# Kernel tuning notes

Measured on AMD Instinct MI355X. Metric: run time of the kernel, lower is better.

Reference implementation:

```python
import jax, jax.numpy as jnp
import numpy as np

WIN = 8          # window size
P = 32           # patch grid side (patch_w_num)
SHIFTS = (0, 4)  # stride=[0,4] -> regular + shifted window branches
HEADS = 16
DH = 64          # dim_head
DIM = 512
HP = HEADS // len(SHIFTS)   # heads per shift branch
NW = (P // WIN) ** 2        # windows per image (16)
WS = WIN * WIN              # tokens per window (64)


def _rel_index():
    c = np.stack(np.meshgrid(np.arange(WIN), np.arange(WIN), indexing="ij")).reshape(2, -1)
    r = (c[:, :, None] - c[:, None, :]).transpose(1, 2, 0) + WIN - 1
    return (r[..., 0] * (2 * WIN - 1) + r[..., 1]).astype(np.int32)  # [WS, WS]

REL_IDX = _rel_index()


def _shift_mask(shift):
    # standard Swin attention mask for cyclic shift
    img = np.zeros((P, P), np.int32); cnt = 0
    sl = (slice(0, -WIN), slice(-WIN, -shift), slice(-shift, None))
    for hs in sl:
        for ws_ in sl:
            img[hs, ws_] = cnt; cnt += 1
    m = img.reshape(P // WIN, WIN, P // WIN, WIN).transpose(0, 2, 1, 3).reshape(NW, WS)
    return np.where(m[:, None, :] != m[:, :, None], -1e9, 0.0).astype(np.float32)  # [NW, WS, WS]

MASK4 = _shift_mask(4)


def _part(t):
    # [B,P,P,hp,dh] -> [B*NW, hp, WS, dh]
    B, _, _, hp, dh = t.shape
    t = t.reshape(B, P // WIN, WIN, P // WIN, WIN, hp, dh)
    t = t.transpose(0, 1, 3, 2, 4, 5, 6).reshape(B * NW, WS, hp, dh)
    return t.transpose(0, 2, 1, 3)


def _merge(t, B):
    # [B*NW, hp, WS, dh] -> [B,P,P,hp,dh]
    hp, dh = t.shape[1], t.shape[3]
    t = t.transpose(0, 2, 1, 3).reshape(B, P // WIN, P // WIN, WIN, WIN, hp, dh)
    return t.transpose(0, 1, 3, 2, 4, 5, 6).reshape(B, P, P, hp, dh)


def setup_inputs() -> dict:
    key = jax.random.key(0)
    ks = jax.random.split(key, 5)
    B = 64
    x = jax.random.normal(ks[0], (B, P * P, DIM), jnp.float32)
    w_qkv = jax.random.normal(ks[1], (DIM, 3 * HEADS * DH), jnp.float32) * (DIM ** -0.5)
    bias_table = jax.random.normal(ks[2], ((2 * WIN - 1) ** 2, HEADS), jnp.float32) * 0.02
    w_out = jax.random.normal(ks[3], (HEADS * DH, DIM), jnp.float32) * ((HEADS * DH) ** -0.5)
    b_out = jnp.zeros((DIM,), jnp.float32)
    return {"x": x, "w_qkv": w_qkv, "bias_table": bias_table, "w_out": w_out, "b_out": b_out}


def reference(x, w_qkv, bias_table, w_out, b_out):
    B, N, _ = x.shape
    scale = DH ** -0.5
    qkv = (x @ w_qkv).reshape(B, P, P, 3, HEADS, DH)
    q, k, v = qkv[..., 0, :, :], qkv[..., 1, :, :], qkv[..., 2, :, :]  # [B,P,P,HEADS,DH]
    bias = bias_table[REL_IDX].transpose(2, 0, 1)  # [HEADS, WS, WS]
    mask4 = jnp.asarray(MASK4)
    outs = []
    for i, shift in enumerate(SHIFTS):
        hs = slice(i * HP, (i + 1) * HP)
        qi, ki, vi = q[..., hs, :], k[..., hs, :], v[..., hs, :]
        if shift:
            qi = jnp.roll(qi, (-shift, -shift), axis=(1, 2))
            ki = jnp.roll(ki, (-shift, -shift), axis=(1, 2))
            vi = jnp.roll(vi, (-shift, -shift), axis=(1, 2))
        qw, kw, vw = _part(qi), _part(ki), _part(vi)  # [B*NW, HP, WS, DH]
        attn = jnp.einsum("whid,whjd->whij", qw * scale, kw) + bias[hs][None]
        if shift:
            attn = attn.reshape(B, NW, HP, WS, WS) + mask4[None, :, None]
            attn = attn.reshape(B * NW, HP, WS, WS)
        attn = jax.nn.softmax(attn, axis=-1)
        ow = jnp.einsum("whij,whjd->whid", attn, vw)
        oi = _merge(ow, B)
        if shift:
            oi = jnp.roll(oi, (shift, shift), axis=(1, 2))
        outs.append(oi)
    out = jnp.concatenate(outs, axis=3).reshape(B, N, HEADS * DH)
    return out @ w_out + b_out
```

## Files before the change

### kernel.cpp

```cpp
#include <hip/hip_runtime.h>
#include <hip/hip_bf16.h>


typedef __attribute__((ext_vector_type(4))) float f32x4;
typedef __attribute__((ext_vector_type(8))) __bf16 bf16x8;
typedef __attribute__((ext_vector_type(8))) unsigned short u16x8;

__device__ __forceinline__ unsigned short f2bf(float f) {
  __hip_bfloat16 h = __float2bfloat16(f);
  return __builtin_bit_cast(unsigned short, h);
}
__device__ __forceinline__ float bf2f(unsigned short u) {
  return __builtin_bit_cast(float, ((unsigned int)u) << 16);
}

#define GLL16(gsrc, ldst)                                                              \
  __builtin_amdgcn_global_load_lds((const __attribute__((address_space(1))) void*)(gsrc), \
                                   (__attribute__((address_space(3))) void*)(ldst), 16, 0, 0)

__global__ __launch_bounds__(256) void cvt_x_kernel(const float* __restrict__ in,
                                                    unsigned short* __restrict__ out, int n4) {
  int i = blockIdx.x * blockDim.x + threadIdx.x;
  int stride = gridDim.x * blockDim.x;
  for (; i < n4; i += stride) {
    float4 v = reinterpret_cast<const float4*>(in)[i];
    ushort4 o;
    o.x = f2bf(v.x); o.y = f2bf(v.y); o.z = f2bf(v.z); o.w = f2bf(v.w);
    reinterpret_cast<ushort4*>(out)[i] = o;
  }
}

__global__ __launch_bounds__(256) void cvt_T_kernel(const float* __restrict__ in,
                                                    unsigned short* __restrict__ out,
                                                    int R, int C) {
  int idx = blockIdx.x * 256 + threadIdx.x;
  if (idx < R * C) {
    int r = idx / C, c = idx - r * C;
    out[(size_t)c * R + r] = f2bf(in[idx]);
  }
}

template <bool OUT_BF16>
__global__ __launch_bounds__(256) void gemm_bt(const unsigned short* __restrict__ A, int lda,
                                               const unsigned short* __restrict__ B, int ldb,
                                               void* __restrict__ Cv, int ldc,
                                               const float* __restrict__ bias,
                                               int N, int K) {
  __shared__ alignas(16) unsigned short As[128 * 32];
  __shared__ alignas(16) unsigned short Bs[128 * 32];
  const int tid = threadIdx.x;
  const int lane = tid & 63;
  const int wave = tid >> 6;
  const int nbn = N >> 7;
  const int nwg = gridDim.x;
  const int b0 = blockIdx.x;
  const int swz = (b0 & 7) * (nwg >> 3) + (b0 >> 3);
  const int bm = swz / nbn, bn = swz - bm * nbn;
  const int m0 = bm << 7, n0 = bn << 7;
  const int wm = (wave >> 1) << 6;
  const int wn = (wave & 1) << 6;
  const int r0 = lane & 15, kh = lane >> 4;

  const int e0 = (wave * 2 + 0) * 512 + lane * 8;
  const int e1 = (wave * 2 + 1) * 512 + lane * 8;
  const int ra0 = e0 >> 5, ca0 = e0 & 31;
  const int ra1 = e1 >> 5, ca1 = e1 & 31;

  f32x4 acc[4][4] = {};
  const int nkt = K >> 5;
  for (int kt = 0; kt < nkt; ++kt) {
    const int k0 = kt << 5;
    if (kt) __syncthreads();
    GLL16(A + (size_t)(m0 + ra0) * lda + k0 + ca0, &As[(wave * 2 + 0) * 512]);
    GLL16(A + (size_t)(m0 + ra1) * lda + k0 + ca1, &As[(wave * 2 + 1) * 512]);
    GLL16(B + (size_t)(n0 + ra0) * ldb + k0 + ca0, &Bs[(wave * 2 + 0) * 512]);
    GLL16(B + (size_t)(n0 + ra1) * ldb + k0 + ca1, &Bs[(wave * 2 + 1) * 512]);
    __syncthreads();
    bf16x8 af[4], bfr[4];
#pragma unroll
    for (int mi = 0; mi < 4; ++mi)
      af[mi] = *reinterpret_cast<const bf16x8*>(&As[(wm + mi * 16 + r0) * 32 + kh * 8]);
#pragma unroll
    for (int ni = 0; ni < 4; ++ni)
      bfr[ni] = *reinterpret_cast<const bf16x8*>(&Bs[(wn + ni * 16 + r0) * 32 + kh * 8]);
#pragma unroll
    for (int mi = 0; mi < 4; ++mi)
#pragma unroll
      for (int ni = 0; ni < 4; ++ni)
        acc[mi][ni] =
            __builtin_amdgcn_mfma_f32_16x16x32_bf16(af[mi], bfr[ni], acc[mi][ni], 0, 0, 0);
  }
  const int rr = kh << 2;
#pragma unroll
  for (int mi = 0; mi < 4; ++mi)
#pragma unroll
    for (int ni = 0; ni < 4; ++ni) {
      const int col = n0 + wn + ni * 16 + r0;
#pragma unroll
      for (int r = 0; r < 4; ++r) {
        const size_t row = (size_t)(m0 + wm + mi * 16 + rr + r);
        if (OUT_BF16)
          ((unsigned short*)Cv)[row * ldc + col] = f2bf(acc[mi][ni][r]);
        else
          ((float*)Cv)[row * ldc + col] = acc[mi][ni][r] + bias[col];
      }
    }
}

__device__ __forceinline__ int region_of(int wy, int wx, int t) {
  int yr = wy * 8 + (t >> 3);
  int xr = wx * 8 + (t & 7);
  int ry = (yr < 24) ? 0 : ((yr < 28) ? 1 : 2);
  int rx = (xr < 24) ? 0 : ((xr < 28) ? 1 : 2);
  return ry * 3 + rx;
}

__global__ __launch_bounds__(256) void win_attn(const unsigned short* __restrict__ qkv,
                                                const float* __restrict__ bias_table,
                                                unsigned short* __restrict__ out,
                                                int nb16) {
  __shared__ alignas(16) unsigned short vt[4][64][72];
  __shared__ alignas(16) unsigned short pl[4][64][72];
  __shared__ unsigned short bias_sh[225 * 16];

  const int tid = threadIdx.x, lane = tid & 63, wave = tid >> 6;
  const int bid = blockIdx.x;
  const int g = bid / nb16;
  const int bw = bid - g * nb16;
  const int b = bw >> 4, w = bw & 15;
  const int wy = w >> 2, wx = w & 3;
  const int shift = g ? 4 : 0;

  for (int i = tid; i < 225 * 16; i += 256) bias_sh[i] = f2bf(bias_table[i]);
  __syncthreads();

  const int r0 = lane & 15, hi4 = lane >> 4;

  for (int hh = 0; hh < 2; ++hh) {
    const int head = g * 8 + wave * 2 + hh;
    const int qcol = head * 64;

    bf16x8 qf[4][2], kf[4][2];
#pragma unroll
    for (int mi = 0; mi < 4; ++mi) {
      const int t = mi * 16 + r0;
      const int y = (wy * 8 + (t >> 3) + shift) & 31;
      const int x = (wx * 8 + (t & 7) + shift) & 31;
      const size_t base = (size_t)((b << 10) + (y << 5) + x) * 3072 + qcol;
#pragma unroll
      for (int kb = 0; kb < 2; ++kb) {
        const int d = kb * 32 + hi4 * 8;
        qf[mi][kb] = *reinterpret_cast<const bf16x8*>(&qkv[base + d]);
        kf[mi][kb] = *reinterpret_cast<const bf16x8*>(&qkv[base + 1024 + d]);
      }
    }

    {
      const int y = (wy * 8 + (lane >> 3) + shift) & 31;
      const int x = (wx * 8 + (lane & 7) + shift) & 31;
      const unsigned short* vsrc =
          qkv + (size_t)((b << 10) + (y << 5) + x) * 3072 + 2048 + qcol;
#pragma unroll
      for (int d0 = 0; d0 < 8; ++d0) {
        u16x8 vv = *reinterpret_cast<const u16x8*>(&vsrc[d0 * 8]);
#pragma unroll
        for (int jj = 0; jj < 8; ++jj) vt[wave][d0 * 8 + jj][lane] = vv[jj];
      }
    }

    f32x4 s[4][4] = {};
#pragma unroll
    for (int mi = 0; mi < 4; ++mi)
#pragma unroll
      for (int ni = 0; ni < 4; ++ni) {
        s[mi][ni] = __builtin_amdgcn_mfma_f32_16x16x32_bf16(qf[mi][0], kf[ni][0], s[mi][ni], 0, 0, 0);
        s[mi][ni] = __builtin_amdgcn_mfma_f32_16x16x32_bf16(qf[mi][1], kf[ni][1], s[mi][ni], 0, 0, 0);
      }

    int rj[4];
#pragma unroll
    for (int ni = 0; ni < 4; ++ni) rj[ni] = region_of(wy, wx, ni * 16 + r0);
    float rinv[4][4];
#pragma unroll
    for (int mi = 0; mi < 4; ++mi) {
#pragma unroll
      for (int r = 0; r < 4; ++r) {
        const int it = mi * 16 + hi4 * 4 + r;
        const int iy = it >> 3, ix = it & 7;
        const int ri = region_of(wy, wx, it);
        float vals[4], vmax = -1e30f;
#pragma unroll
        for (int ni = 0; ni < 4; ++ni) {
          const int jt = ni * 16 + r0;
          const int ridx = (iy - (jt >> 3) + 7) * 15 + (ix - (jt & 7) + 7);
          float v = s[mi][ni][r] * 0.125f + bf2f(bias_sh[ridx * 16 + head]);
          if (g && ri != rj[ni]) v = -1e9f;
          vals[ni] = v;
          vmax = fmaxf(vmax, v);
        }
        vmax = fmaxf(vmax, __shfl_xor(vmax, 1));
        vmax = fmaxf(vmax, __shfl_xor(vmax, 2));
        vmax = fmaxf(vmax, __shfl_xor(vmax, 4));
        vmax = fmaxf(vmax, __shfl_xor(vmax, 8));
        float ssum = 0.f;
#pragma unroll
        for (int ni = 0; ni < 4; ++ni) {
          float p = __expf(vals[ni] - vmax);
          ssum += p;
          s[mi][ni][r] = p;
        }
        ssum += __shfl_xor(ssum, 1);
        ssum += __shfl_xor(ssum, 2);
        ssum += __shfl_xor(ssum, 4);
        ssum += __shfl_xor(ssum, 8);
        rinv[mi][r] = 1.0f / ssum;
      }
    }

#pragma unroll
    for (int mi = 0; mi < 4; ++mi)
#pragma unroll
      for (int ni = 0; ni < 4; ++ni)
#pragma unroll
        for (int r = 0; r < 4; ++r)
          pl[wave][mi * 16 + hi4 * 4 + r][ni * 16 + r0] = f2bf(s[mi][ni][r]);

    f32x4 o[4][4] = {};
#pragma unroll
    for (int kb = 0; kb < 2; ++kb) {
      bf16x8 pf[4], vf[4];
#pragma unroll
      for (int mi = 0; mi < 4; ++mi)
        pf[mi] = *reinterpret_cast<const bf16x8*>(&pl[wave][mi * 16 + r0][kb * 32 + hi4 * 8]);
#pragma unroll
      for (int di = 0; di < 4; ++di)
        vf[di] = *reinterpret_cast<const bf16x8*>(&vt[wave][di * 16 + r0][kb * 32 + hi4 * 8]);
#pragma unroll
      for (int mi = 0; mi < 4; ++mi)
#pragma unroll
        for (int di = 0; di < 4; ++di)
          o[mi][di] = __builtin_amdgcn_mfma_f32_16x16x32_bf16(pf[mi], vf[di], o[mi][di], 0, 0, 0);
    }

#pragma unroll
    for (int mi = 0; mi < 4; ++mi)
#pragma unroll
      for (int r = 0; r < 4; ++r) {
        const int it = mi * 16 + hi4 * 4 + r;
        const int y = (wy * 8 + (it >> 3) + shift) & 31;
        const int x = (wx * 8 + (it & 7) + shift) & 31;
        unsigned short* op = out + (size_t)((b << 10) + (y << 5) + x) * 3072 + head * 64;
        const float rv = rinv[mi][r];
#pragma unroll
        for (int di = 0; di < 4; ++di) op[di * 16 + r0] = f2bf(o[mi][di][r] * rv);
      }
  }
}

extern "C" void kernel_launch(void* const* d_in, const int* in_sizes, int n_in,
                              void* d_out, int out_size, void* d_ws, size_t ws_size,
                              hipStream_t stream) {
  const float* x = (const float*)d_in[0];
  const float* w_qkv = (const float*)d_in[1];
  const float* bias_table = (const float*)d_in[2];
  const float* w_out = (const float*)d_in[3];
  const float* b_out = (const float*)d_in[4];
  float* out = (float*)d_out;

  int S = 1;
  for (; S < 16; S <<= 1) {
    size_t need = 2ull * (2097152ull + 234881024ull / (size_t)S);
    if (need <= ws_size) break;
  }
  const int Mc = 65536 / S;
  const int nb = 64 / S;

  unsigned short* wqt = (unsigned short*)d_ws;
  unsigned short* wot = wqt + (size_t)1572864;
  unsigned short* xb  = wot + (size_t)524288;
  unsigned short* qkv = xb + (size_t)Mc * 512;

  cvt_T_kernel<<<6144, 256, 0, stream>>>(w_qkv, wqt, 512, 3072);
  cvt_T_kernel<<<2048, 256, 0, stream>>>(w_out, wot, 1024, 512);

  for (int c = 0; c < S; ++c) {
    const float* xc = x + (size_t)c * Mc * 512;
    cvt_x_kernel<<<2048, 256, 0, stream>>>(xc, xb, Mc * 128);
    gemm_bt<true><<<(Mc >> 7) * 24, 256, 0, stream>>>(xb, 512, wqt, 512, (void*)qkv, 3072,
                                                      nullptr, 3072, 512);
    win_attn<<<2 * nb * 16, 256, 0, stream>>>(qkv, bias_table, qkv, nb * 16);
    gemm_bt<false><<<(Mc >> 7) * 4, 256, 0, stream>>>(qkv, 3072, wot, 1024,
                                                      (void*)(out + (size_t)c * Mc * 512), 512,
                                                      b_out, 512, 1024);
  }
}
```

Before: 648.4 us.

## Replace GEMM with 256x256 tile, 8-wave, double-buffered pipelined kernel

Replaces the simple 128x128 single-buffered GEMM with a 256x256-tile, 512-thread kernel. It uses a 64-wide K step, double-buffered LDS with XOR swizzling, staged global-to-LDS prefetches interleaved with MFMA phases, and s_setprio around the math. The aim is to raise data reuse, overlap memory loads with compute, and avoid LDS bank conflicts in both projection GEMMs. In exchange it uses 128KB of LDS per block and fewer, larger blocks, which could lower occupancy and raise tail effects on small chunks. The ordering of waitcnt and barriers is delicate.

Result: faster. 592.4 us (-8.6%).

```diff
diff --git a/kernel.cpp b/kernel.cpp
--- a/kernel.cpp
+++ b/kernel.cpp
@@ -17,6 +17,10 @@
 #define GLL16(gsrc, ldst)                                                              \
   __builtin_amdgcn_global_load_lds((const __attribute__((address_space(1))) void*)(gsrc), \
                                    (__attribute__((address_space(3))) void*)(ldst), 16, 0, 0)
+
+#define SWZ(x) ((x) ^ ((((x) >> 9) & 1) << 5))
+
+#define MFMA_BF16 __builtin_amdgcn_mfma_f32_16x16x32_bf16
 
 __global__ __launch_bounds__(256) void cvt_x_kernel(const float* __restrict__ in,
                                                     unsigned short* __restrict__ out, int n4) {
@@ -41,64 +45,143 @@
 }
 
 template <bool OUT_BF16>
-__global__ __launch_bounds__(256) void gemm_bt(const unsigned short* __restrict__ A, int lda,
-                                               const unsigned short* __restrict__ B, int ldb,
-                                               void* __restrict__ Cv, int ldc,
-                                               const float* __restrict__ bias,
-                                               int N, int K) {
-  __shared__ alignas(16) unsigned short As[128 * 32];
-  __shared__ alignas(16) unsigned short Bs[128 * 32];
-  const int tid = threadIdx.x;
-  const int lane = tid & 63;
-  const int wave = tid >> 6;
-  const int nbn = N >> 7;
+__global__ __launch_bounds__(512, 2) void gemm8p(const unsigned short* __restrict__ A, int lda,
+                                                 const unsigned short* __restrict__ B, int ldb,
+                                                 void* __restrict__ Cv, int ldc,
+                                                 const float* __restrict__ bias, int N, int K) {
+  __shared__ alignas(16) unsigned char lds[131072];
+  const int tid = threadIdx.x, lane = tid & 63, wave = tid >> 6;
+  const int wm = wave >> 2, wn = wave & 3;
+  const int nbn = N >> 8;
   const int nwg = gridDim.x;
   const int b0 = blockIdx.x;
-  const int swz = (b0 & 7) * (nwg >> 3) + (b0 >> 3);
-  const int bm = swz / nbn, bn = swz - bm * nbn;
-  const int m0 = bm << 7, n0 = bn << 7;
-  const int wm = (wave >> 1) << 6;
-  const int wn = (wave & 1) << 6;
-  const int r0 = lane & 15, kh = lane >> 4;
-
-  const int e0 = (wave * 2 + 0) * 512 + lane * 8;
-  const int e1 = (wave * 2 + 1) * 512 + lane * 8;
-  const int ra0 = e0 >> 5, ca0 = e0 & 31;
-  const int ra1 = e1 >> 5, ca1 = e1 & 31;
-
-  f32x4 acc[4][4] = {};
-  const int nkt = K >> 5;
-  for (int kt = 0; kt < nkt; ++kt) {
-    const int k0 = kt << 5;
-    if (kt) __syncthreads();
-    GLL16(A + (size_t)(m0 + ra0) * lda + k0 + ca0, &As[(wave * 2 + 0) * 512]);
-    GLL16(A + (size_t)(m0 + ra1) * lda + k0 + ca1, &As[(wave * 2 + 1) * 512]);
-    GLL16(B + (size_t)(n0 + ra0) * ldb + k0 + ca0, &Bs[(wave * 2 + 0) * 512]);
-    GLL16(B + (size_t)(n0 + ra1) * ldb + k0 + ca1, &Bs[(wave * 2 + 1) * 512]);
-    __syncthreads();
-    bf16x8 af[4], bfr[4];
-#pragma unroll
-    for (int mi = 0; mi < 4; ++mi)
-      af[mi] = *reinterpret_cast<const bf16x8*>(&As[(wm + mi * 16 + r0) * 32 + kh * 8]);
-#pragma unroll
-    for (int ni = 0; ni < 4; ++ni)
-      bfr[ni] = *reinterpret_cast<const bf16x8*>(&Bs[(wn + ni * 16 + r0) * 32 + kh * 8]);
-#pragma unroll
-    for (int mi = 0; mi < 4; ++mi)
-#pragma unroll
-      for (int ni = 0; ni < 4; ++ni)
-        acc[mi][ni] =
-            __builtin_amdgcn_mfma_f32_16x16x32_bf16(af[mi], bfr[ni], acc[mi][ni], 0, 0, 0);
-  }
-  const int rr = kh << 2;
-#pragma unroll
-  for (int mi = 0; mi < 4; ++mi)
+  const int sb = (b0 & 7) * (nwg >> 3) + (b0 >> 3);
+  const int bm = sb / nbn, bn = sb - bm * nbn;
+  const int m0 = bm << 8, n0 = bn << 8;
+  const int nkt = K >> 6;
+
+  const int d0 = wave * 1024 + lane * 16;
+  const int r0g = d0 >> 7;
+  const int c0 = (SWZ(d0) & 127) >> 1;
+  const int d1 = d0 + 8192;
+  const int r1g = d1 >> 7;
+  const int c1 = (SWZ(d1) & 127) >> 1;
+
+  const int fr = lane & 15, fk = lane >> 4;
+  const int fkb = fk * 16;
+
+  auto STAGE = [&](const unsigned short* __restrict__ S, int ld, int rbase, int h, int kt,
+                   int bufo, int breg) {
+    const unsigned short* s0 = S + (size_t)(rbase + h * 128 + r0g) * ld + kt * 64 + c0;
+    const unsigned short* s1 = S + (size_t)(rbase + h * 128 + r1g) * ld + kt * 64 + c1;
+    auto* lb = &lds[breg + bufo + h * 16384 + wave * 1024];
+    GLL16(s0, lb);
+    GLL16(s1, lb + 8192);
+  };
+  auto LDA_ = [&](int bufo, int mi, int kb) -> bf16x8 {
+    const int e = (mi * 16 + fr) * 128 + kb * 64 + fkb;
+    return *reinterpret_cast<const bf16x8*>(&lds[bufo + wm * 16384 + SWZ(e)]);
+  };
+  auto LDB_ = [&](int bufo, int ni, int kb) -> bf16x8 {
+    const int e = ((wn & 1) * 64 + ni * 16 + fr) * 128 + kb * 64 + fkb;
+    return *reinterpret_cast<const bf16x8*>(&lds[65536 + bufo + (wn >> 1) * 16384 + SWZ(e)]);
+  };
+
+  STAGE(A, lda, m0, 0, 0, 0, 0);
+  STAGE(A, lda, m0, 1, 0, 0, 0);
+  STAGE(B, ldb, n0, 0, 0, 0, 65536);
+  STAGE(B, ldb, n0, 1, 0, 0, 65536);
+  {
+    const int k1 = (nkt > 1) ? 1 : 0;
+    STAGE(B, ldb, n0, 0, k1, 32768, 65536);
+    STAGE(B, ldb, n0, 1, k1, 32768, 65536);
+  }
+  asm volatile("s_waitcnt vmcnt(4)" ::: "memory");
+  __builtin_amdgcn_s_barrier();
+
+  f32x4 acc[8][4] = {};
+  bf16x8 Af[4][2], Bf[4][2];
+
+  for (int u = 0; u < nkt; ++u) {
+    const int bufo = (u & 1) * 32768;
+    const int bnx = ((u + 1) & 1) * 32768;
+    const int kA = (u + 1 < nkt) ? u + 1 : nkt - 1;
+    const int kB = (u + 2 < nkt) ? u + 2 : nkt - 1;
+
+#pragma unroll
+    for (int mi = 0; mi < 4; ++mi) { Af[mi][0] = LDA_(bufo, mi, 0); Af[mi][1] = LDA_(bufo, mi, 1); }
+#pragma unroll
+    for (int ni = 0; ni < 2; ++ni) { Bf[ni][0] = LDB_(bufo, ni, 0); Bf[ni][1] = LDB_(bufo, ni, 1); }
+    STAGE(A, lda, m0, 0, kA, bnx, 0);
+    __builtin_amdgcn_s_barrier();
+    asm volatile("s_waitcnt lgkmcnt(0)" ::: "memory");
+    __builtin_amdgcn_s_setprio(1);
+#pragma unroll
+    for (int mi = 0; mi < 4; ++mi)
+#pragma unroll
+      for (int ni = 0; ni < 2; ++ni) {
+        acc[mi][ni] = MFMA_BF16(Af[mi][0], Bf[ni][0], acc[mi][ni], 0, 0, 0);
+        acc[mi][ni] = MFMA_BF16(Af[mi][1], Bf[ni][1], acc[mi][ni], 0, 0, 0);
+      }
+    __builtin_amdgcn_s_setprio(0);
+    __builtin_amdgcn_s_barrier();
+
+#pragma unroll
+    for (int ni = 2; ni < 4; ++ni) { Bf[ni][0] = LDB_(bufo, ni, 0); Bf[ni][1] = LDB_(bufo, ni, 1); }
+    STAGE(A, lda, m0, 1, kA, bnx, 0);
+    __builtin_amdgcn_s_barrier();
+    asm volatile("s_waitcnt lgkmcnt(0)" ::: "memory");
+    __builtin_amdgcn_s_setprio(1);
+#pragma unroll
+    for (int mi = 0; mi < 4; ++mi)
+#pragma unroll
+      for (int ni = 2; ni < 4; ++ni) {
+        acc[mi][ni] = MFMA_BF16(Af[mi][0], Bf[ni][0], acc[mi][ni], 0, 0, 0);
+        acc[mi][ni] = MFMA_BF16(Af[mi][1], Bf[ni][1], acc[mi][ni], 0, 0, 0);
+      }
+    __builtin_amdgcn_s_setprio(0);
+    __builtin_amdgcn_s_barrier();
+
+#pragma unroll
+    for (int mi = 0; mi < 4; ++mi) { Af[mi][0] = LDA_(bufo, 4 + mi, 0); Af[mi][1] = LDA_(bufo, 4 + mi, 1); }
+    STAGE(B, ldb, n0, 0, kB, bufo, 65536);
+    __builtin_amdgcn_s_barrier();
+    asm volatile("s_waitcnt lgkmcnt(0)" ::: "memory");
+    __builtin_amdgcn_s_setprio(1);
+#pragma unroll
+    for (int mi = 0; mi < 4; ++mi)
+#pragma unroll
+      for (int ni = 0; ni < 2; ++ni) {
+        acc[4 + mi][ni] = MFMA_BF16(Af[mi][0], Bf[ni][0], acc[4 + mi][ni], 0, 0, 0);
+        acc[4 + mi][ni] = MFMA_BF16(Af[mi][1], Bf[ni][1], acc[4 + mi][ni], 0, 0, 0);
+      }
+    __builtin_amdgcn_s_setprio(0);
+    __builtin_amdgcn_s_barrier();
+
+    STAGE(B, ldb, n0, 1, kB, bufo, 65536);
+    asm volatile("s_waitcnt vmcnt(4)" ::: "memory");
+    __builtin_amdgcn_s_barrier();
+    __builtin_amdgcn_s_setprio(1);
+#pragma unroll
+    for (int mi = 0; mi < 4; ++mi)
+#pragma unroll
+      for (int ni = 2; ni < 4; ++ni) {
+        acc[4 + mi][ni] = MFMA_BF16(Af[mi][0], Bf[ni][0], acc[4 + mi][ni], 0, 0, 0);
+        acc[4 + mi][ni] = MFMA_BF16(Af[mi][1], Bf[ni][1], acc[4 + mi][ni], 0, 0, 0);
+      }
+    __builtin_amdgcn_s_setprio(0);
+    __builtin_amdgcn_s_barrier();
+  }
+
+  const int er = fk << 2;
+#pragma unroll
+  for (int mi = 0; mi < 8; ++mi)
 #pragma unroll
     for (int ni = 0; ni < 4; ++ni) {
-      const int col = n0 + wn + ni * 16 + r0;
+      const int col = n0 + wn * 64 + ni * 16 + fr;
 #pragma unroll
       for (int r = 0; r < 4; ++r) {
-        const size_t row = (size_t)(m0 + wm + mi * 16 + rr + r);
+        const size_t row = (size_t)(m0 + wm * 128 + mi * 16 + er + r);
         if (OUT_BF16)
           ((unsigned short*)Cv)[row * ldc + col] = f2bf(acc[mi][ni][r]);
         else
@@ -173,8 +256,8 @@
     for (int mi = 0; mi < 4; ++mi)
 #pragma unroll
       for (int ni = 0; ni < 4; ++ni) {
-        s[mi][ni] = __builtin_amdgcn_mfma_f32_16x16x32_bf16(qf[mi][0], kf[ni][0], s[mi][ni], 0, 0, 0);
-        s[mi][ni] = __builtin_amdgcn_mfma_f32_16x16x32_bf16(qf[mi][1], kf[ni][1], s[mi][ni], 0, 0, 0);
+        s[mi][ni] = MFMA_BF16(qf[mi][0], kf[ni][0], s[mi][ni], 0, 0, 0);
+        s[mi][ni] = MFMA_BF16(qf[mi][1], kf[ni][1], s[mi][ni], 0, 0, 0);
       }
 
     int rj[4];
@@ -239,7 +322,7 @@
       for (int mi = 0; mi < 4; ++mi)
 #pragma unroll
         for (int di = 0; di < 4; ++di)
-          o[mi][di] = __builtin_amdgcn_mfma_f32_16x16x32_bf16(pf[mi], vf[di], o[mi][di], 0, 0, 0);
+          o[mi][di] = MFMA_BF16(pf[mi], vf[di], o[mi][di], 0, 0, 0);
     }
 
 #pragma unroll
@@ -286,11 +369,11 @@
   for (int c = 0; c < S; ++c) {
     const float* xc = x + (size_t)c * Mc * 512;
     cvt_x_kernel<<<2048, 256, 0, stream>>>(xc, xb, Mc * 128);
-    gemm_bt<true><<<(Mc >> 7) * 24, 256, 0, stream>>>(xb, 512, wqt, 512, (void*)qkv, 3072,
-                                                      nullptr, 3072, 512);
+    gemm8p<true><<<(Mc >> 8) * 12, 512, 0, stream>>>(xb, 512, wqt, 512, (void*)qkv, 3072,
+                                                     nullptr, 3072, 512);
     win_attn<<<2 * nb * 16, 256, 0, stream>>>(qkv, bias_table, qkv, nb * 16);
-    gemm_bt<false><<<(Mc >> 7) * 4, 256, 0, stream>>>(qkv, 3072, wot, 1024,
-                                                      (void*)(out + (size_t)c * Mc * 512), 512,
-                                                      b_out, 512, 1024);
-  }
-}
+    gemm8p<false><<<(Mc >> 8) * 2, 512, 0, stream>>>(qkv, 3072, wot, 1024,
+                                                     (void*)(out + (size_t)c * Mc * 512), 512,
+                                                     b_out, 512, 1024);
+  }
+}
```
